# Optimization experiments

Hardware: AMD Instinct MI355X
Metric: run time of the kernel (lower is better)

The kernel has to match this reference:

```python
import jax, jax.numpy as jnp
import numpy as np

D_MODEL = 2048
N_HEADS = 16
HEAD_DIM = D_MODEL // N_HEADS
D_FF = 8192


def setup_inputs() -> dict:
    key = jax.random.key(0)
    ks = jax.random.split(key, 16)
    s = 0.02
    inp = {
        'x': jax.random.normal(ks[0], (2, 2048, D_MODEL), dtype=jnp.float32),
        'Wq': jax.random.normal(ks[1], (D_MODEL, D_MODEL), jnp.float32) * s,
        'bq': jnp.zeros((D_MODEL,), jnp.float32),
        'Wk': jax.random.normal(ks[2], (D_MODEL, D_MODEL), jnp.float32) * s,
        'bk': jnp.zeros((D_MODEL,), jnp.float32),
        'Wv': jax.random.normal(ks[3], (D_MODEL, D_MODEL), jnp.float32) * s,
        'bv': jnp.zeros((D_MODEL,), jnp.float32),
        'Wo': jax.random.normal(ks[4], (D_MODEL, D_MODEL), jnp.float32) * s,
        'bo': jnp.zeros((D_MODEL,), jnp.float32),
        'rotary': jax.random.normal(ks[5], (1, 1, HEAD_DIM), jnp.float32) * s,
        'norm1_w': jnp.ones((D_MODEL,), jnp.float32),
        'norm2_w': jnp.ones((D_MODEL,), jnp.float32),
        'W1': jax.random.normal(ks[6], (2 * D_FF, D_MODEL), jnp.float32) * s,
        'b1': jnp.zeros((2 * D_FF,), jnp.float32),
        'W2': jax.random.normal(ks[7], (D_MODEL, D_FF), jnp.float32) * s,
        'b2': jnp.zeros((D_MODEL,), jnp.float32),
    }
    return inp


def _rmsnorm(x, w, eps=1e-8):
    return w * (x * jax.lax.rsqrt(jnp.mean(x * x, axis=-1, keepdims=True) + eps))


def reference(x, Wq, bq, Wk, bk, Wv, bv, Wo, bo, rotary, norm1_w, norm2_w, W1, b1, W2, b2):
    B, S, _ = x.shape
    # --- attention block ---
    h = _rmsnorm(x, norm1_w)
    q = (h @ Wq.T + bq).reshape(B, S, N_HEADS, HEAD_DIM)
    k = (h @ Wk.T + bk).reshape(B, S, N_HEADS, HEAD_DIM)
    v = (h @ Wv.T + bv).reshape(B, S, N_HEADS, HEAD_DIM)
    q = q + rotary  # (1,1,head_dim) broadcast over batch, seq, heads
    scores = jnp.einsum('bqhd,bkhd->bhqk', q, k) / jnp.sqrt(jnp.float32(HEAD_DIM))
    attn = jax.nn.softmax(scores, axis=-1)
    o = jnp.einsum('bhqk,bkhd->bqhd', attn, v).reshape(B, S, D_MODEL)
    x = x + (o @ Wo.T + bo)
    # --- SwiGLU FFN block ---
    h2 = _rmsnorm(x, norm2_w)
    g = h2 @ W1.T + b1
    x1, x2 = g[..., :D_FF], g[..., D_FF:]
    ff = (x1 * jax.nn.silu(x2)) @ W2.T + b2
    return x + ff
```

## Files before the change

### kernel.cpp

```cpp
#include <hip/hip_runtime.h>
#include <hip/hip_bf16.h>

#define D_MODEL 2048
#define N_HEADS 16
#define HEAD_DIM 128
#define D_FF 8192
#define BATCH 2
#define SEQ 2048
#define M_TOK (BATCH * SEQ)
#define QKV_LD 6144
#define QSCALE 0.12751744f

typedef __attribute__((ext_vector_type(8))) short short8;
typedef __attribute__((ext_vector_type(4))) short short4v;
typedef __attribute__((ext_vector_type(4))) float f32x4;
typedef __attribute__((ext_vector_type(16))) float f32x16;
typedef __attribute__((ext_vector_type(2))) unsigned int uint2v;
typedef __attribute__((ext_vector_type(4))) unsigned int uint4v;

__device__ __forceinline__ unsigned short f2b(float f) {
  __hip_bfloat16 h = __float2bfloat16(f);
  return *reinterpret_cast<unsigned short*>(&h);
}
__device__ __forceinline__ float b2f(unsigned short u) {
  unsigned int x = ((unsigned int)u) << 16;
  return __uint_as_float(x);
}

__device__ __forceinline__ void gload_lds16(const void* gsrc, void* ldst) {
  __builtin_amdgcn_global_load_lds(
      (const __attribute__((address_space(1))) void*)gsrc,
      (__attribute__((address_space(3))) void*)ldst, 16, 0, 0);
}

__device__ __forceinline__ f32x16 mfma32(short8 a, short8 b, f32x16 c) {
  return __builtin_amdgcn_mfma_f32_32x32x16_bf16(a, b, c, 0, 0, 0);
}
__device__ __forceinline__ unsigned int cvtpk(float lo, float hi) {
  unsigned int r;
  asm("v_cvt_pk_bf16_f32 %0, %1, %2" : "=v"(r) : "v"(lo), "v"(hi));
  return r;
}
__device__ __forceinline__ uint2v plswap(unsigned int a, unsigned int b) {
  return __builtin_amdgcn_permlane32_swap(a, b, false, false);
}

__global__ __launch_bounds__(256)
void cvt_kernel(const float* __restrict__ src, unsigned short* __restrict__ dst,
                int nchunks, float scale) {
  int i = blockIdx.x * blockDim.x + threadIdx.x;
  int stride = gridDim.x * blockDim.x;
  for (int c = i; c < nchunks; c += stride) {
    const float4 a = *(const float4*)(src + (size_t)c * 8);
    const float4 b = *(const float4*)(src + (size_t)c * 8 + 4);
    short8 r;
    r[0] = f2b(a.x * scale); r[1] = f2b(a.y * scale);
    r[2] = f2b(a.z * scale); r[3] = f2b(a.w * scale);
    r[4] = f2b(b.x * scale); r[5] = f2b(b.y * scale);
    r[6] = f2b(b.z * scale); r[7] = f2b(b.w * scale);
    *(short8*)(dst + (size_t)c * 8) = r;
  }
}

__global__ void biasqkv_kernel(const float* __restrict__ bq,
                               const float* __restrict__ bk,
                               const float* __restrict__ bv,
                               const float* __restrict__ rot,
                               float* __restrict__ outp) {
  int i = blockIdx.x * 256 + threadIdx.x;
  float v;
  if (i < 2048) v = (bq[i] + rot[i & (HEAD_DIM - 1)]) * QSCALE;
  else if (i < 4096) v = bk[i - 2048];
  else v = bv[i - 4096];
  outp[i] = v;
}

__global__ __launch_bounds__(256)
void rmsnorm_kernel(const float* __restrict__ x, const float* __restrict__ wv,
                    unsigned short* __restrict__ outp) {
  const int row = blockIdx.x;
  const float* xr = x + (size_t)row * D_MODEL;
  const int base = threadIdx.x * 8;
  float4 a = *(const float4*)(xr + base);
  float4 c = *(const float4*)(xr + base + 4);
  float ss = a.x * a.x + a.y * a.y + a.z * a.z + a.w * a.w +
             c.x * c.x + c.y * c.y + c.z * c.z + c.w * c.w;
#pragma unroll
  for (int m = 1; m < 64; m <<= 1) ss += __shfl_xor(ss, m);
  __shared__ float red[4];
  if ((threadIdx.x & 63) == 0) red[threadIdx.x >> 6] = ss;
  __syncthreads();
  float tot = red[0] + red[1] + red[2] + red[3];
  float sc = rsqrtf(tot * (1.0f / D_MODEL) + 1e-8f);
  float4 w0 = *(const float4*)(wv + base);
  float4 w1 = *(const float4*)(wv + base + 4);
  short8 r;
  r[0] = f2b(a.x * sc * w0.x); r[1] = f2b(a.y * sc * w0.y);
  r[2] = f2b(a.z * sc * w0.z); r[3] = f2b(a.w * sc * w0.w);
  r[4] = f2b(c.x * sc * w1.x); r[5] = f2b(c.y * sc * w1.y);
  r[6] = f2b(c.z * sc * w1.z); r[7] = f2b(c.w * sc * w1.w);
  *(short8*)(outp + (size_t)row * D_MODEL + base) = r;
}

template <int MODE>
__global__ __launch_bounds__(512, 2)
void gemm_p8(const unsigned short* __restrict__ A, int lda,
             const unsigned short* __restrict__ W, int ldw,
             const float* __restrict__ bias, void* __restrict__ outp,
             int N, int K, size_t out_zstride) {
  __shared__ unsigned short AL[2][2][128 * 64];
  __shared__ unsigned short BL[2][2][128 * 64];
  const int t = threadIdx.x;
  const int l = t & 63, w = t >> 6;
  const int wm = w >> 2, wn = w & 3;
  const int ln = l & 31, hi = l >> 5;
  const int m0 = blockIdx.y << 8, n0 = blockIdx.x << 8;
  const int koff = blockIdx.z * K;

  const int r0 = t >> 3;
  const int cb16 = (t & 7) * 16;
  const int sel = ((cb16 ^ ((r0 & 7) << 4)) >> 1);
  const unsigned short* Abase = A + (size_t)m0 * lda + koff;
  const unsigned short* Wbase = W + (size_t)n0 * ldw + koff;
  const int d0e = t * 8, d1e = (t + 512) * 8;

#define STAGE(XL, Xb, ld, dd, h, ktd)                                        \
  do {                                                                       \
    const unsigned short* s_ =                                               \
        (Xb) + (size_t)((h) * 128 + r0) * (ld) + (ktd) * 64 + sel;           \
    gload_lds16(s_, &XL[dd][h][d0e]);                                        \
    gload_lds16(s_ + (size_t)64 * (ld), &XL[dd][h][d1e]);                    \
  } while (0)

  const int swz = (ln & 7) << 4;
  const int hb = wn >> 1;
  const int browb = ((wn & 1) * 64 + ln) * 128;

  f32x16 acc[4][2] = {};
  short8 bf[2][4];

#define READB(dd)                                                            \
  do {                                                                       \
    const char* Bb_ = (const char*)&BL[dd][hb][0];                           \
    _Pragma("unroll") for (int cb_ = 0; cb_ < 2; cb_++)                      \
      _Pragma("unroll") for (int ks_ = 0; ks_ < 4; ks_++)                    \
        bf[cb_][ks_] = *(const short8*)(Bb_ + browb + cb_ * 4096 +           \
                                        ((ks_ * 32 + hi * 16) ^ swz));       \
  } while (0)

#define PHASE(dd, rb, RB, STAGE_STMT, VM_STMT)                               \
  do {                                                                       \
    const char* Ab_ = (const char*)&AL[dd][(rb) >> 1][0];                    \
    short8 af_[4];                                                           \
    if (RB) READB(dd);                                                       \
    _Pragma("unroll") for (int ks_ = 0; ks_ < 4; ks_++)                      \
      af_[ks_] = *(const short8*)(Ab_ +                                      \
                                  (wm * 64 + ((rb) & 1) * 32 + ln) * 128 +   \
                                  ((ks_ * 32 + hi * 16) ^ swz));             \
    STAGE_STMT;                                                              \
    __builtin_amdgcn_sched_barrier(0);                                       \
    VM_STMT;                                                                 \
    __builtin_amdgcn_sched_barrier(0);                                       \
    __builtin_amdgcn_s_barrier();                                            \
    __builtin_amdgcn_sched_barrier(0);                                       \
    __builtin_amdgcn_s_setprio(1);                                           \
    _Pragma("unroll") for (int cb_ = 0; cb_ < 2; cb_++)                      \
      _Pragma("unroll") for (int ks_ = 0; ks_ < 4; ks_++)                    \
        acc[rb][cb_] = mfma32(af_[ks_], bf[cb_][ks_], acc[rb][cb_]);         \
    __builtin_amdgcn_s_setprio(0);                                           \
    __builtin_amdgcn_sched_barrier(0);                                       \
    __builtin_amdgcn_s_barrier();                                            \
    __builtin_amdgcn_sched_barrier(0);                                       \
  } while (0)

  const int NT = K >> 6;

  STAGE(AL, Abase, lda, 0, 0, 0);
  STAGE(AL, Abase, lda, 0, 1, 0);
  STAGE(BL, Wbase, ldw, 0, 0, 0);
  STAGE(BL, Wbase, ldw, 0, 1, 0);
  STAGE(AL, Abase, lda, 1, 0, 1);
  STAGE(BL, Wbase, ldw, 1, 0, 1);
  asm volatile("s_waitcnt vmcnt(4)" ::: "memory");
  __builtin_amdgcn_sched_barrier(0);
  __builtin_amdgcn_s_barrier();
  __builtin_amdgcn_sched_barrier(0);

  for (int kt = 0; kt < NT; kt += 2) {
    PHASE(0, 0, 1,
          { if (kt + 1 < NT) STAGE(BL, Wbase, ldw, 1, 1, kt + 1); }, {});
    PHASE(0, 1, 0,
          { if (kt + 1 < NT) STAGE(AL, Abase, lda, 1, 1, kt + 1); }, {});
    PHASE(0, 2, 0,
          { if (kt + 2 < NT) STAGE(AL, Abase, lda, 0, 0, kt + 2); }, {});
    PHASE(0, 3, 0,
          { if (kt + 2 < NT) STAGE(BL, Wbase, ldw, 0, 0, kt + 2); },
          {
            if (kt + 2 < NT)
              asm volatile("s_waitcnt vmcnt(4)" ::: "memory");
            else
              asm volatile("s_waitcnt vmcnt(0)" ::: "memory");
          });
    PHASE(1, 0, 1,
          { if (kt + 2 < NT) STAGE(BL, Wbase, ldw, 0, 1, kt + 2); }, {});
    PHASE(1, 1, 0,
          { if (kt + 2 < NT) STAGE(AL, Abase, lda, 0, 1, kt + 2); }, {});
    PHASE(1, 2, 0,
          { if (kt + 3 < NT) STAGE(AL, Abase, lda, 1, 0, kt + 3); }, {});
    PHASE(1, 3, 0,
          { if (kt + 3 < NT) STAGE(BL, Wbase, ldw, 1, 0, kt + 3); },
          {
            if (kt + 3 < NT)
              asm volatile("s_waitcnt vmcnt(4)" ::: "memory");
            else
              asm volatile("s_waitcnt vmcnt(0)" ::: "memory");
          });
  }
#undef PHASE
#undef READB
#undef STAGE

#pragma unroll
  for (int rb = 0; rb < 4; rb++)
#pragma unroll
    for (int cb = 0; cb < 2; cb++) {
      const int col = n0 + wn * 64 + cb * 32 + ln;
      const float bv = (MODE == 0) ? bias[col] : 0.0f;
      const int rowb = m0 + (rb >> 1) * 128 + wm * 64 + (rb & 1) * 32 + 4 * hi;
#pragma unroll
      for (int r = 0; r < 16; r++) {
        const int row = rowb + (r & 3) + 8 * (r >> 2);
        const float vv = acc[rb][cb][r] + bv;
        if (MODE == 0)
          ((unsigned short*)outp)[(size_t)row * N + col] = f2b(vv);
        else
          ((float*)outp + blockIdx.z * out_zstride)[(size_t)row * N + col] = vv;
      }
    }
}

template <int MODE>
__global__ __launch_bounds__(256)
void gemm_bt(const unsigned short* __restrict__ A, int lda,
             const unsigned short* __restrict__ W, int ldw,
             const float* __restrict__ bias, const float* res, void* outp,
             int N, int K, size_t out_zstride) {
  __shared__ unsigned short As[128 * 32];
  __shared__ unsigned short Bs[128 * 32];
  const int t = threadIdx.x;
  const int l = t & 63;
  const int w = t >> 6;
  const int m0 = blockIdx.y << 7;
  const int n0 = blockIdx.x << 7;
  const int wr = (w >> 1) << 6;
  const int wc = (w & 1) << 6;
  const int koff = blockIdx.z * K;

  const unsigned short* Ab = A + (size_t)m0 * lda + koff;
  const unsigned short* Wb = W + (size_t)n0 * ldw + koff;

  f32x4 acc[4][4] = {};

  const int c0 = t, c1 = t + 256;
  const int ar0 = c0 >> 2, ak0 = (c0 & 3) * 8;
  const int ar1 = c1 >> 2, ak1 = (c1 & 3) * 8;
  const int lr = l & 15, lk = (l >> 4) * 8;

  for (int k0 = 0; k0 < K; k0 += 32) {
    gload_lds16(Ab + (size_t)ar0 * lda + k0 + ak0, &As[c0 * 8]);
    gload_lds16(Ab + (size_t)ar1 * lda + k0 + ak1, &As[c1 * 8]);
    gload_lds16(Wb + (size_t)ar0 * ldw + k0 + ak0, &Bs[c0 * 8]);
    gload_lds16(Wb + (size_t)ar1 * ldw + k0 + ak1, &Bs[c1 * 8]);
    __syncthreads();
    short8 a[4], b[4];
#pragma unroll
    for (int mi = 0; mi < 4; mi++)
      a[mi] = *(const short8*)&As[(wr + mi * 16 + lr) * 32 + lk];
#pragma unroll
    for (int ni = 0; ni < 4; ni++)
      b[ni] = *(const short8*)&Bs[(wc + ni * 16 + lr) * 32 + lk];
#pragma unroll
    for (int mi = 0; mi < 4; mi++)
#pragma unroll
      for (int ni = 0; ni < 4; ni++)
        acc[mi][ni] = __builtin_amdgcn_mfma_f32_16x16x32_bf16(
            a[mi], b[ni], acc[mi][ni], 0, 0, 0);
    __syncthreads();
  }

  const int lg = (l >> 4) * 4;
#pragma unroll
  for (int mi = 0; mi < 4; mi++) {
#pragma unroll
    for (int ni = 0; ni < 4; ni++) {
      int cn = n0 + wc + ni * 16 + lr;
      float bval = bias[cn];
#pragma unroll
      for (int j = 0; j < 4; j++) {
        int r = m0 + wr + mi * 16 + lg + j;
        float vv = acc[mi][ni][j] + bval;
        size_t idx = (size_t)r * N + cn;
        ((float*)outp)[idx] = vv + res[idx];
      }
    }
  }
  (void)out_zstride;
}

__global__ __launch_bounds__(256)
void vtrans_kernel(const unsigned short* __restrict__ qkv,
                   unsigned short* __restrict__ vt) {
  const int bh = blockIdx.y;
  const int b = bh >> 4, h = bh & 15;
  const int s0 = blockIdx.x * 32;
  __shared__ unsigned short tile[32][136];
  const int t = threadIdx.x;
  for (int i = 0; i < 2; i++) {
    int c = t + i * 256;
    int s = c >> 4, dc = c & 15;
    *(short8*)&tile[s][dc * 8] =
        *(const short8*)(qkv + (size_t)(b * SEQ + s0 + s) * QKV_LD + 4096 +
                         h * HEAD_DIM + dc * 8);
  }
  __syncthreads();
  const int d = t >> 1, sh = (t & 1) * 16;
  unsigned short* dst = vt + ((size_t)bh * HEAD_DIM + d) * SEQ + s0 + sh;
  short8 r0, r1;
#pragma unroll
  for (int j = 0; j < 8; j++) r0[j] = tile[sh + j][d];
#pragma unroll
  for (int j = 0; j < 8; j++) r1[j] = tile[sh + 8 + j][d];
  *(short8*)dst = r0;
  *(short8*)(dst + 8) = r1;
}

__global__ __launch_bounds__(512, 2)
void attn_kernel(const unsigned short* __restrict__ qkv,
                 const unsigned short* __restrict__ vt,
                 unsigned short* __restrict__ o) {
  const int bh = blockIdx.y;
  const int b = bh >> 4, h = bh & 15;
  const int q0 = blockIdx.x << 8;
  const int t = threadIdx.x, w = t >> 6, l = t & 63;
  const int ln = l & 31, hi = l >> 5;

  __shared__ unsigned short Ks[2][64 * 128];

  short8 qf[8];
  {
    const unsigned short* qb =
        qkv + (size_t)(b * SEQ + q0 + w * 32 + ln) * QKV_LD + h * HEAD_DIM +
        hi * 8;
#pragma unroll
    for (int sl = 0; sl < 8; sl++) qf[sl] = *(const short8*)(qb + sl * 16);
  }

  f32x16 oacc[4] = {};
  float mrow = -1e30f, lrow = 0.f;

  const unsigned short* kbase =
      qkv + (size_t)(b * SEQ) * QKV_LD + 2048 + h * HEAD_DIM;
  const unsigned short* vbase = vt + (size_t)bh * HEAD_DIM * SEQ;

#define STAGEK(buf, kv0_)                                                    \
  do {                                                                       \
    _Pragma("unroll") for (int i_ = 0; i_ < 2; i_++) {                       \
      int c_ = t + i_ * 512;                                                 \
      int row_ = c_ >> 4, dc_ = c_ & 15;                                     \
      int sel_ = ((dc_ * 16) ^ ((row_ & 7) << 4)) >> 1;                      \
      gload_lds16(kbase + (size_t)((kv0_) + row_) * QKV_LD + sel_,           \
                  &Ks[buf][c_ * 8]);                                         \
    }                                                                        \
  } while (0)

  STAGEK(0, 0);
  __syncthreads();

  for (int it = 0; it < SEQ / 64; ++it) {
    const int cur = it & 1;
    const int kv0 = it * 64;

    short8 vf[4][4];
#pragma unroll
    for (int db = 0; db < 4; db++)
#pragma unroll
      for (int ks = 0; ks < 4; ks++)
        vf[db][ks] = *(const short8*)(vbase + (size_t)(db * 32 + ln) * SEQ +
                                      kv0 + ks * 16 + hi * 8);

    if (it + 1 < SEQ / 64) STAGEK(cur ^ 1, kv0 + 64);

    const char* kb = (const char*)&Ks[cur][0];
    f32x16 s0 = {}, s1 = {};
#pragma unroll
    for (int sl = 0; sl < 8; sl++) {
      const int cw = (sl * 32 + hi * 16) ^ ((ln & 7) << 4);
      short8 kf0 = *(const short8*)(kb + ln * 256 + cw);
      short8 kf1 = *(const short8*)(kb + (32 + ln) * 256 + cw);
      s0 = mfma32(kf0, qf[sl], s0);
      s1 = mfma32(kf1, qf[sl], s1);
    }

    float mx = s0[0];
#pragma unroll
    for (int r = 1; r < 16; r++) mx = fmaxf(mx, s0[r]);
#pragma unroll
    for (int r = 0; r < 16; r++) mx = fmaxf(mx, s1[r]);
    {
      uint2v r2 = plswap(__float_as_uint(mx), __float_as_uint(mx));
      mx = fmaxf(__uint_as_float(r2[0]), __uint_as_float(r2[1]));
    }

    if (!__all(mx <= mrow + 8.f)) {
      float mnew = fmaxf(mrow, mx);
      float fs = exp2f(mrow - mnew);
      mrow = mnew;
      lrow *= fs;
#pragma unroll
      for (int db = 0; db < 4; db++)
#pragma unroll
        for (int r = 0; r < 16; r++) oacc[db][r] *= fs;
    }

    float p0[16], p1[16];
    float sum = 0.f;
#pragma unroll
    for (int r = 0; r < 16; r++) {
      p0[r] = exp2f(s0[r] - mrow);
      sum += p0[r];
    }
#pragma unroll
    for (int r = 0; r < 16; r++) {
      p1[r] = exp2f(s1[r] - mrow);
      sum += p1[r];
    }
    lrow += sum;

    uint4v pk[4];
#define PACKSUB(P, K0)                                                       \
  {                                                                          \
    unsigned int a_, b_;                                                     \
    uint2v r_;                                                               \
    a_ = cvtpk(P[0], P[1]); b_ = cvtpk(P[4], P[5]);                          \
    r_ = plswap(a_, b_); pk[K0][0] = r_[0]; pk[K0][2] = r_[1];               \
    a_ = cvtpk(P[2], P[3]); b_ = cvtpk(P[6], P[7]);                          \
    r_ = plswap(a_, b_); pk[K0][1] = r_[0]; pk[K0][3] = r_[1];               \
    a_ = cvtpk(P[8], P[9]); b_ = cvtpk(P[12], P[13]);                        \
    r_ = plswap(a_, b_); pk[K0 + 1][0] = r_[0]; pk[K0 + 1][2] = r_[1];       \
    a_ = cvtpk(P[10], P[11]); b_ = cvtpk(P[14], P[15]);                      \
    r_ = plswap(a_, b_); pk[K0 + 1][1] = r_[0]; pk[K0 + 1][3] = r_[1];       \
  }
    PACKSUB(p0, 0);
    PACKSUB(p1, 2);
#undef PACKSUB

#pragma unroll
    for (int db = 0; db < 4; db++)
#pragma unroll
      for (int ks = 0; ks < 4; ks++)
        oacc[db] = mfma32(vf[db][ks], __builtin_bit_cast(short8, pk[ks]),
                          oacc[db]);

    __syncthreads();
  }
#undef STAGEK

  {
    uint2v r2 = plswap(__float_as_uint(lrow), __float_as_uint(lrow));
    lrow = __uint_as_float(r2[0]) + __uint_as_float(r2[1]);
  }
  const float inv = 1.0f / lrow;
  unsigned short* ob = o + (size_t)(b * SEQ + q0 + w * 32 + ln) * D_MODEL +
                       h * HEAD_DIM + hi * 4;
#pragma unroll
  for (int db = 0; db < 4; db++)
#pragma unroll
    for (int r = 0; r < 4; r++) {
      short4v v4;
#pragma unroll
      for (int j = 0; j < 4; j++)
        v4[j] = (short)f2b(oacc[db][4 * r + j] * inv);
      *(short4v*)(ob + db * 32 + r * 8) = v4;
    }
}

__global__ __launch_bounds__(256)
void swiglu_kernel(unsigned short* __restrict__ g) {
  size_t i = (size_t)blockIdx.x * 256 + threadIdx.x;
  size_t m = i >> 10, jc = i & 1023;
  unsigned short* p1 = g + m * (2 * D_FF) + jc * 8;
  short8 aa = *(short8*)p1;
  short8 bb = *(short8*)(p1 + D_FF);
  short8 r;
#pragma unroll
  for (int jj = 0; jj < 8; jj++) {
    float x1 = b2f((unsigned short)aa[jj]);
    float x2 = b2f((unsigned short)bb[jj]);
    float sg = x2 / (1.0f + __expf(-x2));
    r[jj] = f2b(x1 * sg);
  }
  *(short8*)p1 = r;
}

__global__ __launch_bounds__(256)
void reduce2_kernel(const float* __restrict__ p0, const float* __restrict__ p1,
                    const float* __restrict__ b2, float* __restrict__ out) {
  size_t i = (size_t)blockIdx.x * 256 + threadIdx.x;
  float4 a = ((const float4*)p0)[i];
  float4 b = ((const float4*)p1)[i];
  float4 o = ((const float4*)out)[i];
  float4 bb = ((const float4*)b2)[i & 511];
  o.x += a.x + b.x + bb.x;
  o.y += a.y + b.y + bb.y;
  o.z += a.z + b.z + bb.z;
  o.w += a.w + b.w + bb.w;
  ((float4*)out)[i] = o;
}

extern "C" void kernel_launch(void* const* d_in, const int* in_sizes, int n_in,
                              void* d_out, int out_size, void* d_ws,
                              size_t ws_size, hipStream_t stream) {
  (void)in_sizes; (void)n_in; (void)out_size; (void)ws_size;
  const float* x   = (const float*)d_in[0];
  const float* Wq  = (const float*)d_in[1];
  const float* bq  = (const float*)d_in[2];
  const float* Wk  = (const float*)d_in[3];
  const float* bk  = (const float*)d_in[4];
  const float* Wv  = (const float*)d_in[5];
  const float* bv  = (const float*)d_in[6];
  const float* Wo  = (const float*)d_in[7];
  const float* bo  = (const float*)d_in[8];
  const float* rot = (const float*)d_in[9];
  const float* n1w = (const float*)d_in[10];
  const float* n2w = (const float*)d_in[11];
  const float* W1  = (const float*)d_in[12];
  const float* b1  = (const float*)d_in[13];
  const float* W2  = (const float*)d_in[14];
  const float* b2  = (const float*)d_in[15];
  float* out = (float*)d_out;
  char* ws = (char*)d_ws;

  const size_t SZ_D2  = (size_t)D_MODEL * D_MODEL * 2;
  const size_t SZ_ACT = (size_t)M_TOK * D_MODEL * 2;
  const size_t SZ_W1  = (size_t)2 * D_FF * D_MODEL * 2;
  const size_t SZ_W2  = (size_t)D_MODEL * D_FF * 2;
  const size_t SZ_G   = (size_t)M_TOK * 2 * D_FF * 2;

  size_t off = 0;
  auto alloc = [&](size_t sz) { size_t o = off; off += (sz + 255) & ~(size_t)255; return o; };
  unsigned short* wqkv_b = (unsigned short*)(ws + alloc(3 * SZ_D2));
  unsigned short* wo_b   = (unsigned short*)(ws + alloc(SZ_D2));
  unsigned short* w1_b   = (unsigned short*)(ws + alloc(SZ_W1));
  unsigned short* w2_b   = (unsigned short*)(ws + alloc(SZ_W2));
  float*          biasq  = (float*)(ws + alloc(QKV_LD * 4));
  unsigned short* h2_b   = (unsigned short*)(ws + alloc(SZ_ACT));
  char* pool = ws + alloc(SZ_G);
  unsigned short* h_b   = (unsigned short*)(pool);
  unsigned short* qkv_b = (unsigned short*)(pool + SZ_ACT);
  unsigned short* vt_b  = (unsigned short*)(pool + 4 * SZ_ACT);
  unsigned short* o_b   = (unsigned short*)(pool + 5 * SZ_ACT);
  unsigned short* g_b   = (unsigned short*)(pool);
  float* p0 = (float*)ws;
  float* p1 = p0 + (size_t)M_TOK * D_MODEL;

  cvt_kernel<<<1024, 256, 0, stream>>>(Wq, wqkv_b, D_MODEL * D_MODEL / 8, QSCALE);
  cvt_kernel<<<1024, 256, 0, stream>>>(Wk, wqkv_b + (size_t)D_MODEL * D_MODEL, D_MODEL * D_MODEL / 8, 1.0f);
  cvt_kernel<<<1024, 256, 0, stream>>>(Wv, wqkv_b + (size_t)2 * D_MODEL * D_MODEL, D_MODEL * D_MODEL / 8, 1.0f);
  cvt_kernel<<<1024, 256, 0, stream>>>(Wo, wo_b, D_MODEL * D_MODEL / 8, 1.0f);
  cvt_kernel<<<2048, 256, 0, stream>>>(W1, w1_b, 2 * D_FF * D_MODEL / 8, 1.0f);
  cvt_kernel<<<2048, 256, 0, stream>>>(W2, w2_b, D_MODEL * D_FF / 8, 1.0f);
  biasqkv_kernel<<<QKV_LD / 256, 256, 0, stream>>>(bq, bk, bv, rot, biasq);

  rmsnorm_kernel<<<M_TOK, 256, 0, stream>>>(x, n1w, h_b);

  gemm_p8<0><<<dim3(QKV_LD / 256, M_TOK / 256), 512, 0, stream>>>(
      h_b, D_MODEL, wqkv_b, D_MODEL, biasq, qkv_b, QKV_LD, D_MODEL, 0);

  vtrans_kernel<<<dim3(SEQ / 32, BATCH * N_HEADS), 256, 0, stream>>>(qkv_b, vt_b);
  attn_kernel<<<dim3(SEQ / 256, BATCH * N_HEADS), 512, 0, stream>>>(qkv_b, vt_b, o_b);

  gemm_bt<1><<<dim3(D_MODEL / 128, M_TOK / 128), 256, 0, stream>>>(
      o_b, D_MODEL, wo_b, D_MODEL, bo, x, out, D_MODEL, D_MODEL, 0);

  rmsnorm_kernel<<<M_TOK, 256, 0, stream>>>(out, n2w, h2_b);

  gemm_p8<0><<<dim3(2 * D_FF / 256, M_TOK / 256), 512, 0, stream>>>(
      h2_b, D_MODEL, w1_b, D_MODEL, b1, g_b, 2 * D_FF, D_MODEL, 0);

  swiglu_kernel<<<(M_TOK * D_FF / 8) / 256, 256, 0, stream>>>(g_b);

  gemm_p8<2><<<dim3(D_MODEL / 256, M_TOK / 256, 2), 512, 0, stream>>>(
      g_b, 2 * D_FF, w2_b, D_FF, nullptr, p0, D_MODEL, D_FF / 2,
      (size_t)M_TOK * D_MODEL);

  reduce2_kernel<<<(M_TOK * D_MODEL / 4) / 256, 256, 0, stream>>>(p0, p1, b2, out);
}
```

Baseline: 955.2 us.

## Fuse SwiGLU into W1 GEMM epilogue via interleaved weights and change LDS swizzle

During weight conversion, W1 rows and b1 are permuted so that each 64-column tile holds 32 gate columns and their 32 matching value columns. The W1 GEMM epilogue can then apply SiLU gating in registers and write a half-width bf16 FF activation. This removes the standalone SwiGLU kernel and the write and re-read of the full 2*D_FF intermediate. The LDS XOR swizzle in the GEMM and attention K tile also changes to mix in row>>3, meant to reduce bank conflicts, at the cost of slightly more index arithmetic.

```diff
diff --git a/kernel.cpp b/kernel.cpp
--- a/kernel.cpp
+++ b/kernel.cpp
@@ -62,6 +62,33 @@
   }
 }
 
+__global__ __launch_bounds__(256)
+void cvt_w1p_kernel(const float* __restrict__ src,
+                    unsigned short* __restrict__ dst) {
+  int i = blockIdx.x * blockDim.x + threadIdx.x;
+  int stride = gridDim.x * blockDim.x;
+  const int total = 2 * D_FF * (D_MODEL / 8);
+  for (int c = i; c < total; c += stride) {
+    int rp = c >> 8, col8 = c & 255;
+    int b = rp >> 6, half = (rp >> 5) & 1;
+    int rs = half * D_FF + b * 32 + (rp & 31);
+    const float* s = src + (size_t)rs * D_MODEL + col8 * 8;
+    const float4 a = *(const float4*)s;
+    const float4 bb = *(const float4*)(s + 4);
+    short8 r;
+    r[0] = f2b(a.x); r[1] = f2b(a.y); r[2] = f2b(a.z); r[3] = f2b(a.w);
+    r[4] = f2b(bb.x); r[5] = f2b(bb.y); r[6] = f2b(bb.z); r[7] = f2b(bb.w);
+    *(short8*)(dst + (size_t)c * 8) = r;
+  }
+}
+
+__global__ void permb1_kernel(const float* __restrict__ b1,
+                              float* __restrict__ b1p) {
+  int i = blockIdx.x * 256 + threadIdx.x;
+  int b = i >> 6, half = (i >> 5) & 1;
+  b1p[i] = b1[half * D_FF + b * 32 + (i & 31)];
+}
+
 __global__ void biasqkv_kernel(const float* __restrict__ bq,
                                const float* __restrict__ bk,
                                const float* __restrict__ bv,
@@ -119,7 +146,8 @@
 
   const int r0 = t >> 3;
   const int cb16 = (t & 7) * 16;
-  const int sel = ((cb16 ^ ((r0 & 7) << 4)) >> 1);
+  const int fs = ((r0 + (r0 >> 3)) & 7) << 4;
+  const int sel = ((cb16 ^ fs) >> 1);
   const unsigned short* Abase = A + (size_t)m0 * lda + koff;
   const unsigned short* Wbase = W + (size_t)n0 * ldw + koff;
   const int d0e = t * 8, d1e = (t + 512) * 8;
@@ -132,9 +160,9 @@
     gload_lds16(s_ + (size_t)64 * (ld), &XL[dd][h][d1e]);                    \
   } while (0)
 
-  const int swz = (ln & 7) << 4;
   const int hb = wn >> 1;
   const int browb = ((wn & 1) * 64 + ln) * 128;
+  const int lnf = ln + (ln >> 3);
 
   f32x16 acc[4][2] = {};
   short8 bf[2][4];
@@ -142,21 +170,24 @@
 #define READB(dd)                                                            \
   do {                                                                       \
     const char* Bb_ = (const char*)&BL[dd][hb][0];                           \
-    _Pragma("unroll") for (int cb_ = 0; cb_ < 2; cb_++)                      \
+    _Pragma("unroll") for (int cb_ = 0; cb_ < 2; cb_++) {                    \
+      const int fb_ = ((lnf + 4 * cb_) & 7) << 4;                            \
       _Pragma("unroll") for (int ks_ = 0; ks_ < 4; ks_++)                    \
         bf[cb_][ks_] = *(const short8*)(Bb_ + browb + cb_ * 4096 +           \
-                                        ((ks_ * 32 + hi * 16) ^ swz));       \
+                                        ((ks_ * 32 + hi * 16) ^ fb_));       \
+    }                                                                        \
   } while (0)
 
 #define PHASE(dd, rb, RB, STAGE_STMT, VM_STMT)                               \
   do {                                                                       \
     const char* Ab_ = (const char*)&AL[dd][(rb) >> 1][0];                    \
+    const int fa_ = ((lnf + 4 * ((rb) & 1)) & 7) << 4;                       \
     short8 af_[4];                                                           \
     if (RB) READB(dd);                                                       \
     _Pragma("unroll") for (int ks_ = 0; ks_ < 4; ks_++)                      \
       af_[ks_] = *(const short8*)(Ab_ +                                      \
                                   (wm * 64 + ((rb) & 1) * 32 + ln) * 128 +   \
-                                  ((ks_ * 32 + hi * 16) ^ swz));             \
+                                  ((ks_ * 32 + hi * 16) ^ fa_));             \
     STAGE_STMT;                                                              \
     __builtin_amdgcn_sched_barrier(0);                                       \
     VM_STMT;                                                                 \
@@ -221,22 +252,38 @@
 #undef STAGE
 
 #pragma unroll
-  for (int rb = 0; rb < 4; rb++)
-#pragma unroll
-    for (int cb = 0; cb < 2; cb++) {
-      const int col = n0 + wn * 64 + cb * 32 + ln;
-      const float bv = (MODE == 0) ? bias[col] : 0.0f;
-      const int rowb = m0 + (rb >> 1) * 128 + wm * 64 + (rb & 1) * 32 + 4 * hi;
+  for (int rb = 0; rb < 4; rb++) {
+    const int rowb = m0 + (rb >> 1) * 128 + wm * 64 + (rb & 1) * 32 + 4 * hi;
+    if (MODE == 3) {
+      const int col0 = n0 + wn * 64 + ln;
+      const float b1v = bias[col0];
+      const float b2v = bias[col0 + 32];
+      const int jout = (n0 >> 1) + wn * 32 + ln;
 #pragma unroll
       for (int r = 0; r < 16; r++) {
         const int row = rowb + (r & 3) + 8 * (r >> 2);
-        const float vv = acc[rb][cb][r] + bv;
-        if (MODE == 0)
-          ((unsigned short*)outp)[(size_t)row * N + col] = f2b(vv);
-        else
-          ((float*)outp + blockIdx.z * out_zstride)[(size_t)row * N + col] = vv;
+        float x1 = acc[rb][0][r] + b1v;
+        float x2 = acc[rb][1][r] + b2v;
+        float sg = x2 / (1.0f + __expf(-x2));
+        ((unsigned short*)outp)[(size_t)row * (N >> 1) + jout] = f2b(x1 * sg);
       }
-    }
+    } else {
+#pragma unroll
+      for (int cb = 0; cb < 2; cb++) {
+        const int col = n0 + wn * 64 + cb * 32 + ln;
+        const float bv = (MODE == 0) ? bias[col] : 0.0f;
+#pragma unroll
+        for (int r = 0; r < 16; r++) {
+          const int row = rowb + (r & 3) + 8 * (r >> 2);
+          const float vv = acc[rb][cb][r] + bv;
+          if (MODE == 0)
+            ((unsigned short*)outp)[(size_t)row * N + col] = f2b(vv);
+          else
+            ((float*)outp + blockIdx.z * out_zstride)[(size_t)row * N + col] = vv;
+        }
+      }
+    }
+  }
 }
 
 template <int MODE>
@@ -367,7 +414,8 @@
     _Pragma("unroll") for (int i_ = 0; i_ < 2; i_++) {                       \
       int c_ = t + i_ * 512;                                                 \
       int row_ = c_ >> 4, dc_ = c_ & 15;                                     \
-      int sel_ = ((dc_ * 16) ^ ((row_ & 7) << 4)) >> 1;                      \
+      int f_ = ((row_ + (row_ >> 3)) & 7) << 4;                              \
+      int sel_ = ((dc_ * 16) ^ f_) >> 1;                                     \
       gload_lds16(kbase + (size_t)((kv0_) + row_) * QKV_LD + sel_,           \
                   &Ks[buf][c_ * 8]);                                         \
     }                                                                        \
@@ -376,6 +424,9 @@
   STAGEK(0, 0);
   __syncthreads();
 
+  const int f0 = ((ln + (ln >> 3)) & 7) << 4;
+  const int f1 = ((ln + (ln >> 3) + 4) & 7) << 4;
+
   for (int it = 0; it < SEQ / 64; ++it) {
     const int cur = it & 1;
     const int kv0 = it * 64;
@@ -394,9 +445,9 @@
     f32x16 s0 = {}, s1 = {};
 #pragma unroll
     for (int sl = 0; sl < 8; sl++) {
-      const int cw = (sl * 32 + hi * 16) ^ ((ln & 7) << 4);
-      short8 kf0 = *(const short8*)(kb + ln * 256 + cw);
-      short8 kf1 = *(const short8*)(kb + (32 + ln) * 256 + cw);
+      const int cwb = sl * 32 + hi * 16;
+      short8 kf0 = *(const short8*)(kb + ln * 256 + (cwb ^ f0));
+      short8 kf1 = *(const short8*)(kb + (32 + ln) * 256 + (cwb ^ f1));
       s0 = mfma32(kf0, qf[sl], s0);
       s1 = mfma32(kf1, qf[sl], s1);
     }
@@ -482,24 +533,6 @@
         v4[j] = (short)f2b(oacc[db][4 * r + j] * inv);
       *(short4v*)(ob + db * 32 + r * 8) = v4;
     }
-}
-
-__global__ __launch_bounds__(256)
-void swiglu_kernel(unsigned short* __restrict__ g) {
-  size_t i = (size_t)blockIdx.x * 256 + threadIdx.x;
-  size_t m = i >> 10, jc = i & 1023;
-  unsigned short* p1 = g + m * (2 * D_FF) + jc * 8;
-  short8 aa = *(short8*)p1;
-  short8 bb = *(short8*)(p1 + D_FF);
-  short8 r;
-#pragma unroll
-  for (int jj = 0; jj < 8; jj++) {
-    float x1 = b2f((unsigned short)aa[jj]);
-    float x2 = b2f((unsigned short)bb[jj]);
-    float sg = x2 / (1.0f + __expf(-x2));
-    r[jj] = f2b(x1 * sg);
-  }
-  *(short8*)p1 = r;
 }
 
 __global__ __launch_bounds__(256)
@@ -553,13 +586,14 @@
   unsigned short* w1_b   = (unsigned short*)(ws + alloc(SZ_W1));
   unsigned short* w2_b   = (unsigned short*)(ws + alloc(SZ_W2));
   float*          biasq  = (float*)(ws + alloc(QKV_LD * 4));
+  float*          b1p    = (float*)(ws + alloc(2 * D_FF * 4));
   unsigned short* h2_b   = (unsigned short*)(ws + alloc(SZ_ACT));
   char* pool = ws + alloc(SZ_G);
   unsigned short* h_b   = (unsigned short*)(pool);
   unsigned short* qkv_b = (unsigned short*)(pool + SZ_ACT);
   unsigned short* vt_b  = (unsigned short*)(pool + 4 * SZ_ACT);
   unsigned short* o_b   = (unsigned short*)(pool + 5 * SZ_ACT);
-  unsigned short* g_b   = (unsigned short*)(pool);
+  unsigned short* ff_b  = (unsigned short*)(pool);
   float* p0 = (float*)ws;
   float* p1 = p0 + (size_t)M_TOK * D_MODEL;
 
@@ -567,9 +601,10 @@
   cvt_kernel<<<1024, 256, 0, stream>>>(Wk, wqkv_b + (size_t)D_MODEL * D_MODEL, D_MODEL * D_MODEL / 8, 1.0f);
   cvt_kernel<<<1024, 256, 0, stream>>>(Wv, wqkv_b + (size_t)2 * D_MODEL * D_MODEL, D_MODEL * D_MODEL / 8, 1.0f);
   cvt_kernel<<<1024, 256, 0, stream>>>(Wo, wo_b, D_MODEL * D_MODEL / 8, 1.0f);
-  cvt_kernel<<<2048, 256, 0, stream>>>(W1, w1_b, 2 * D_FF * D_MODEL / 8, 1.0f);
+  cvt_w1p_kernel<<<2048, 256, 0, stream>>>(W1, w1_b);
   cvt_kernel<<<2048, 256, 0, stream>>>(W2, w2_b, D_MODEL * D_FF / 8, 1.0f);
   biasqkv_kernel<<<QKV_LD / 256, 256, 0, stream>>>(bq, bk, bv, rot, biasq);
+  permb1_kernel<<<2 * D_FF / 256, 256, 0, stream>>>(b1, b1p);
 
   rmsnorm_kernel<<<M_TOK, 256, 0, stream>>>(x, n1w, h_b);
 
@@ -584,13 +619,11 @@
 
   rmsnorm_kernel<<<M_TOK, 256, 0, stream>>>(out, n2w, h2_b);
 
-  gemm_p8<0><<<dim3(2 * D_FF / 256, M_TOK / 256), 512, 0, stream>>>(
-      h2_b, D_MODEL, w1_b, D_MODEL, b1, g_b, 2 * D_FF, D_MODEL, 0);
-
-  swiglu_kernel<<<(M_TOK * D_FF / 8) / 256, 256, 0, stream>>>(g_b);
+  gemm_p8<3><<<dim3(2 * D_FF / 256, M_TOK / 256), 512, 0, stream>>>(
+      h2_b, D_MODEL, w1_b, D_MODEL, b1p, ff_b, 2 * D_FF, D_MODEL, 0);
 
   gemm_p8<2><<<dim3(D_MODEL / 256, M_TOK / 256, 2), 512, 0, stream>>>(
-      g_b, 2 * D_FF, w2_b, D_FF, nullptr, p0, D_MODEL, D_FF / 2,
+      ff_b, D_FF, w2_b, D_FF, nullptr, p0, D_MODEL, D_FF / 2,
       (size_t)M_TOK * D_MODEL);
 
   reduce2_kernel<<<(M_TOK * D_MODEL / 4) / 256, 256, 0, stream>>>(p0, p1, b2, out);
```

Result: no change. 937.2 us (-1.9%).
